# Performance work log

Measured on AMD Instinct MI355X. Metric: run time of the kernel, lower is better.

## Reference

```python
import jax, jax.numpy as jnp
import numpy as np

BATCH_SIZE = 2048
TEMPERATURE = 0.5
EPS = 1e-8  # torch CosineSimilarity eps


def setup_inputs() -> dict:
    key = jax.random.key(0)
    k1, k2 = jax.random.split(key)
    d = 512
    z_i = jax.random.normal(k1, (BATCH_SIZE, d), dtype=jnp.float32)
    z_j = jax.random.normal(k2, (BATCH_SIZE, d), dtype=jnp.float32)
    return {"z_i": z_i, "z_j": z_j}


def reference(z_i, z_j):
    B = BATCH_SIZE
    n = 2 * B
    z = jnp.concatenate([z_i, z_j], axis=0)              # [n, d]
    # cosine similarity via normalize + GEMM (same math as broadcasted CosineSimilarity)
    norms = jnp.maximum(jnp.linalg.norm(z, axis=1, keepdims=True), EPS)
    zn = z / norms                                       # [n, d]
    S = zn @ zn.T                                        # [n, n]
    # drop diagonal: row i keeps columns j != i, in order (matches sim[~eye].view(n, n-1))
    cols = jnp.arange(n - 1)[None, :]                    # [1, n-1]
    rows = jnp.arange(n)[:, None]                        # [n, 1]
    idx = cols + (cols >= rows)                          # skip diagonal
    off_diag = jnp.take_along_axis(S, idx, axis=1)       # [n, n-1]
    # positive pair: pos_pairs = cat(z_j, z_i) -> partner index (i + B) mod n
    pos = jnp.take_along_axis(S, ((rows[:, 0] + B) % n)[:, None], axis=1)  # [n, 1]
    logits = jnp.concatenate([pos, off_diag], axis=1) / TEMPERATURE        # [n, n]
    # cross-entropy with label 0, reduction='sum', then / n  == mean over rows
    loss = jnp.mean(jax.nn.logsumexp(logits, axis=1) - logits[:, 0])
    return loss
```

## Files before the change

kernel.cpp:

```cpp
#include <hip/hip_runtime.h>
#include <hip/hip_bf16.h>

#define N_TOT 4096
#define D     512
#define BHALF 2048

#define EXP2_SCALE 2.8853900817779268f
#define E2 7.3890560989306495f

typedef __attribute__((ext_vector_type(4))) float floatx4;

#define AS_GLOBAL(p) ((const __attribute__((address_space(1))) void*)(p))
#define AS_LDS(p)    ((__attribute__((address_space(3))) void*)(p))

#define WAITCNT_VM(n) (0xF70 | (n))

__global__ void normalize_kernel(const float* __restrict__ z_i,
                                 const float* __restrict__ z_j,
                                 unsigned char* __restrict__ zn,
                                 float* __restrict__ rowsum) {
    const int wave = threadIdx.x >> 6, lane = threadIdx.x & 63;
    const int row = blockIdx.x * 4 + wave;
    const float* src = (row < BHALF) ? (z_i + (size_t)row * D)
                                     : (z_j + (size_t)(row - BHALF) * D);
    if (lane == 0) rowsum[row] = 0.0f;
    float4 v0 = ((const float4*)src)[lane];
    float4 v1 = ((const float4*)src)[lane + 64];
    float ss = v0.x*v0.x + v0.y*v0.y + v0.z*v0.z + v0.w*v0.w
             + v1.x*v1.x + v1.y*v1.y + v1.z*v1.z + v1.w*v1.w;
    #pragma unroll
    for (int off = 32; off > 0; off >>= 1) ss += __shfl_xor(ss, off);
    float inv = 1.0f / fmaxf(sqrtf(ss), 1e-8f);
    int w0 = __builtin_amdgcn_cvt_pk_fp8_f32(v0.x * inv, v0.y * inv, 0, false);
    w0     = __builtin_amdgcn_cvt_pk_fp8_f32(v0.z * inv, v0.w * inv, w0, true);
    int w1 = __builtin_amdgcn_cvt_pk_fp8_f32(v1.x * inv, v1.y * inv, 0, false);
    w1     = __builtin_amdgcn_cvt_pk_fp8_f32(v1.z * inv, v1.w * inv, w1, true);
    int* dst = (int*)(zn + (size_t)row * D);
    dst[lane]      = w0;
    dst[lane + 64] = w1;
}

__launch_bounds__(256)
__global__ void gemm_fused(const unsigned char* __restrict__ zn,
                           float* __restrict__ rowsum,
                           float* __restrict__ spos) {
    __shared__ unsigned char At[3][128 * 32];
    __shared__ unsigned char Bt[3][128 * 32];

    int b = blockIdx.x, bi = 0, rowlen = 32;
    while (b >= rowlen) { b -= rowlen; rowlen--; bi++; }
    const int bj = bi + b;
    const int i0 = bi * 128;
    const int j0 = bj * 128;

    const int t = threadIdx.x;
    const int lane = t & 63, wave = t >> 6;
    const int wm = wave & 1, wn = wave >> 1;
    const int quad = lane >> 4, l16 = lane & 15;

    const int srow = wave * 32 + (lane >> 1);
    const int scol = (lane & 1) * 16;
    const unsigned char* gA = zn + (size_t)(i0 + srow) * D + scol;
    const unsigned char* gB = zn + (size_t)(j0 + srow) * D + scol;
    const int lo = srow * 32 + scol;

    floatx4 acc[4][4] = {};

    __builtin_amdgcn_global_load_lds(AS_GLOBAL(gA),      AS_LDS(&At[0][lo]), 16, 0, 0);
    __builtin_amdgcn_global_load_lds(AS_GLOBAL(gB),      AS_LDS(&Bt[0][lo]), 16, 0, 0);
    __builtin_amdgcn_global_load_lds(AS_GLOBAL(gA + 32), AS_LDS(&At[1][lo]), 16, 0, 0);
    __builtin_amdgcn_global_load_lds(AS_GLOBAL(gB + 32), AS_LDS(&Bt[1][lo]), 16, 0, 0);

    #pragma unroll
    for (int kt = 0; kt < 16; ++kt) {
        const int cur = kt % 3;
        if (kt < 15) __builtin_amdgcn_s_waitcnt(WAITCNT_VM(2));
        else         __builtin_amdgcn_s_waitcnt(WAITCNT_VM(0));
        __builtin_amdgcn_s_barrier();
        __asm__ volatile("" ::: "memory");
        if (kt < 14) {
            const int nxt = (kt + 2) % 3;
            const int ko = (kt + 2) * 32;
            __builtin_amdgcn_global_load_lds(AS_GLOBAL(gA + ko), AS_LDS(&At[nxt][lo]), 16, 0, 0);
            __builtin_amdgcn_global_load_lds(AS_GLOBAL(gB + ko), AS_LDS(&Bt[nxt][lo]), 16, 0, 0);
        }
        long af[4], bf[4];
        #pragma unroll
        for (int tm = 0; tm < 4; ++tm)
            af[tm] = *(const long*)(&At[cur][(wm*64 + tm*16 + l16) * 32 + quad*8]);
        #pragma unroll
        for (int tn = 0; tn < 4; ++tn)
            bf[tn] = *(const long*)(&Bt[cur][(wn*64 + tn*16 + l16) * 32 + quad*8]);
        #pragma unroll
        for (int tm = 0; tm < 4; ++tm)
            #pragma unroll
            for (int tn = 0; tn < 4; ++tn)
                acc[tm][tn] = __builtin_amdgcn_mfma_f32_16x16x32_fp8_fp8(
                    af[tm], bf[tn], acc[tm][tn], 0, 0, 0);
    }

    float cs[4] = {0.f, 0.f, 0.f, 0.f};
    #pragma unroll
    for (int tm = 0; tm < 4; ++tm) {
        float rs[4] = {0.f, 0.f, 0.f, 0.f};
        #pragma unroll
        for (int tn = 0; tn < 4; ++tn)
            #pragma unroll
            for (int r = 0; r < 4; ++r) {
                float e = exp2f(acc[tm][tn][r] * EXP2_SCALE);
                rs[r] += e;
                cs[tn] += e;
            }
        #pragma unroll
        for (int r = 0; r < 4; ++r) {
            float v = rs[r];
            v += __shfl_xor(v, 1);
            v += __shfl_xor(v, 2);
            v += __shfl_xor(v, 4);
            v += __shfl_xor(v, 8);
            if (l16 == 0) {
                int gi = i0 + wm*64 + tm*16 + quad*4 + r;
                atomicAdd(&rowsum[gi], v);
            }
        }
    }
    if (bi != bj) {
        #pragma unroll
        for (int tn = 0; tn < 4; ++tn) {
            float v = cs[tn];
            v += __shfl_xor(v, 16);
            v += __shfl_xor(v, 32);
            if (quad == 0) {
                int gj = j0 + wn*64 + tn*16 + l16;
                atomicAdd(&rowsum[gj], v);
            }
        }
    }
    if (bj == bi + 16) {
        #pragma unroll
        for (int tm = 0; tm < 4; ++tm)
            #pragma unroll
            for (int tn = 0; tn < 4; ++tn)
                #pragma unroll
                for (int r = 0; r < 4; ++r) {
                    int li = wm*64 + tm*16 + quad*4 + r;
                    int lj = wn*64 + tn*16 + l16;
                    if (li == lj) {
                        float s = acc[tm][tn][r];
                        spos[i0 + li]         = s;
                        spos[i0 + li + BHALF] = s;
                    }
                }
    }
}

__global__ void finalize_kernel(const float* __restrict__ rowsum,
                                const float* __restrict__ spos,
                                float* __restrict__ out) {
    int t = threadIdx.x;
    float acc = 0.f;
    for (int i = t; i < N_TOT; i += 1024) {
        float sp = spos[i];
        float denom = rowsum[i] - E2 + exp2f(sp * EXP2_SCALE);
        acc += __logf(denom) - 2.0f * sp;
    }
    #pragma unroll
    for (int off = 32; off > 0; off >>= 1) acc += __shfl_xor(acc, off);
    __shared__ float red[16];
    if ((t & 63) == 0) red[t >> 6] = acc;
    __syncthreads();
    if (t == 0) {
        float s = 0.f;
        #pragma unroll
        for (int w = 0; w < 16; ++w) s += red[w];
        out[0] = s / (float)N_TOT;
    }
}

extern "C" void kernel_launch(void* const* d_in, const int* in_sizes, int n_in,
                              void* d_out, int out_size, void* d_ws, size_t ws_size,
                              hipStream_t stream) {
    const float* z_i = (const float*)d_in[0];
    const float* z_j = (const float*)d_in[1];
    float* out = (float*)d_out;

    char* ws = (char*)d_ws;
    unsigned char* zn = (unsigned char*)ws;
    float* rowsum = (float*)(ws + (size_t)N_TOT * D);
    float* spos   = rowsum + N_TOT;

    normalize_kernel<<<N_TOT / 4, 256, 0, stream>>>(z_i, z_j, zn, rowsum);
    gemm_fused<<<(32 * 33) / 2, 256, 0, stream>>>(zn, rowsum, spos);
    finalize_kernel<<<1, 1024, 0, stream>>>(rowsum, spos, out);
}
```

Before: 89.80 us.

## Load GEMM fragments directly from global into registers, dropping LDS staging

Replaces the triple-buffered LDS staging (global_load_lds with waitcnt and barriers) with per-lane 8-byte global loads straight into MFMA operand registers, software-pipelined one k-step ahead. This removes LDS traffic and the block-wide barriers. In exchange, each wave re-fetches operand rows that other waves share, relying on L1/L2, and uses narrow 8-byte global accesses with strided rows, which may hurt coalescing and raise global load pressure.

Result: slower. 110.3 us (+22.9%).

```diff
diff --git a/kernel.cpp b/kernel.cpp
--- a/kernel.cpp
+++ b/kernel.cpp
@@ -9,11 +9,6 @@
 #define E2 7.3890560989306495f
 
 typedef __attribute__((ext_vector_type(4))) float floatx4;
-
-#define AS_GLOBAL(p) ((const __attribute__((address_space(1))) void*)(p))
-#define AS_LDS(p)    ((__attribute__((address_space(3))) void*)(p))
-
-#define WAITCNT_VM(n) (0xF70 | (n))
 
 __global__ void normalize_kernel(const float* __restrict__ z_i,
                                  const float* __restrict__ z_j,
@@ -44,9 +39,6 @@
 __global__ void gemm_fused(const unsigned char* __restrict__ zn,
                            float* __restrict__ rowsum,
                            float* __restrict__ spos) {
-    __shared__ unsigned char At[3][128 * 32];
-    __shared__ unsigned char Bt[3][128 * 32];
-
     int b = blockIdx.x, bi = 0, rowlen = 32;
     while (b >= rowlen) { b -= rowlen; rowlen--; bi++; }
     const int bj = bi + b;
@@ -58,45 +50,36 @@
     const int wm = wave & 1, wn = wave >> 1;
     const int quad = lane >> 4, l16 = lane & 15;
 
-    const int srow = wave * 32 + (lane >> 1);
-    const int scol = (lane & 1) * 16;
-    const unsigned char* gA = zn + (size_t)(i0 + srow) * D + scol;
-    const unsigned char* gB = zn + (size_t)(j0 + srow) * D + scol;
-    const int lo = srow * 32 + scol;
+    const unsigned char* pA = zn + (size_t)(i0 + wm*64 + l16) * D + quad*8;
+    const unsigned char* pB = zn + (size_t)(j0 + wn*64 + l16) * D + quad*8;
 
     floatx4 acc[4][4] = {};
+    long a0[4], b0[4], a1[4], b1[4];
 
-    __builtin_amdgcn_global_load_lds(AS_GLOBAL(gA),      AS_LDS(&At[0][lo]), 16, 0, 0);
-    __builtin_amdgcn_global_load_lds(AS_GLOBAL(gB),      AS_LDS(&Bt[0][lo]), 16, 0, 0);
-    __builtin_amdgcn_global_load_lds(AS_GLOBAL(gA + 32), AS_LDS(&At[1][lo]), 16, 0, 0);
-    __builtin_amdgcn_global_load_lds(AS_GLOBAL(gB + 32), AS_LDS(&Bt[1][lo]), 16, 0, 0);
+    #pragma unroll
+    for (int tm = 0; tm < 4; ++tm) a0[tm] = *(const long*)(pA + tm*16*D);
+    #pragma unroll
+    for (int tn = 0; tn < 4; ++tn) b0[tn] = *(const long*)(pB + tn*16*D);
 
     #pragma unroll
     for (int kt = 0; kt < 16; ++kt) {
-        const int cur = kt % 3;
-        if (kt < 15) __builtin_amdgcn_s_waitcnt(WAITCNT_VM(2));
-        else         __builtin_amdgcn_s_waitcnt(WAITCNT_VM(0));
-        __builtin_amdgcn_s_barrier();
-        __asm__ volatile("" ::: "memory");
-        if (kt < 14) {
-            const int nxt = (kt + 2) % 3;
-            const int ko = (kt + 2) * 32;
-            __builtin_amdgcn_global_load_lds(AS_GLOBAL(gA + ko), AS_LDS(&At[nxt][lo]), 16, 0, 0);
-            __builtin_amdgcn_global_load_lds(AS_GLOBAL(gB + ko), AS_LDS(&Bt[nxt][lo]), 16, 0, 0);
+        if (kt < 15) {
+            const int ko = (kt + 1) * 32;
+            #pragma unroll
+            for (int tm = 0; tm < 4; ++tm)
+                a1[tm] = *(const long*)(pA + tm*16*D + ko);
+            #pragma unroll
+            for (int tn = 0; tn < 4; ++tn)
+                b1[tn] = *(const long*)(pB + tn*16*D + ko);
         }
-        long af[4], bf[4];
-        #pragma unroll
-        for (int tm = 0; tm < 4; ++tm)
-            af[tm] = *(const long*)(&At[cur][(wm*64 + tm*16 + l16) * 32 + quad*8]);
-        #pragma unroll
-        for (int tn = 0; tn < 4; ++tn)
-            bf[tn] = *(const long*)(&Bt[cur][(wn*64 + tn*16 + l16) * 32 + quad*8]);
         #pragma unroll
         for (int tm = 0; tm < 4; ++tm)
             #pragma unroll
             for (int tn = 0; tn < 4; ++tn)
                 acc[tm][tn] = __builtin_amdgcn_mfma_f32_16x16x32_fp8_fp8(
-                    af[tm], bf[tn], acc[tm][tn], 0, 0, 0);
+                    a0[tm], b0[tn], acc[tm][tn], 0, 0, 0);
+        #pragma unroll
+        for (int i = 0; i < 4; ++i) { a0[i] = a1[i]; b0[i] = b1[i]; }
     }
 
     float cs[4] = {0.f, 0.f, 0.f, 0.f};
```
